# Kernel tuning notes

Hardware: AMD Instinct MI355X
Metric: run time of the kernel (lower is better)

## Reference

```python
import jax, jax.numpy as jnp
import numpy as np

H = 20  # hidden size (hardcoded in the torch module)

def setup_inputs() -> dict:
    key = jax.random.key(0)
    ks = jax.random.split(key, 7)
    s = 0.1  # keep activations in a sane range for tanh/sigmoid
    return {
        "x":     jax.random.normal(ks[0], (8192, 512, 12), dtype=jnp.float32),
        "w_ih":  jax.random.normal(ks[1], (4 * H, 12), dtype=jnp.float32) * s,
        "w_hh":  jax.random.normal(ks[2], (4 * H, H), dtype=jnp.float32) * s,
        "b_ih":  jax.random.normal(ks[3], (4 * H,), dtype=jnp.float32) * s,
        "b_hh":  jax.random.normal(ks[4], (4 * H,), dtype=jnp.float32) * s,
        "w_out": jax.random.normal(ks[5], (10, H), dtype=jnp.float32) * s,
        "b_out": jax.random.normal(ks[6], (10,), dtype=jnp.float32) * s,
    }

def reference(x, w_ih, w_hh, b_ih, b_hh, w_out, b_out):
    # x: [B, T, I]. Single-layer LSTM (PyTorch gate order i,f,g,o), zero init state,
    # then Linear on the last hidden state.
    B, T, _ = x.shape
    # Precompute input projections for all timesteps: [T, B, 4H]
    x_proj = jnp.einsum('bti,gi->tbg', x, w_ih) + (b_ih + b_hh)

    def step(carry, xt):
        h, c = carry                      # each [B, H]
        gates = xt + h @ w_hh.T           # [B, 4H]
        i, f, g, o = jnp.split(gates, 4, axis=-1)
        i = jax.nn.sigmoid(i)
        f = jax.nn.sigmoid(f)
        g = jnp.tanh(g)
        o = jax.nn.sigmoid(o)
        c = f * c + i * g
        h = o * jnp.tanh(c)
        return (h, c), None

    h0 = jnp.zeros((B, H), dtype=x.dtype)
    c0 = jnp.zeros((B, H), dtype=x.dtype)
    (h_last, _), _ = jax.lax.scan(step, (h0, c0), x_proj)
    # out = Linear(h_T): r_out[:, -1, :] == h_n for a single-layer LSTM
    return h_last @ w_out.T + b_out
```

## Files before the change

kernel.cpp:

```cpp
#include <hip/hip_runtime.h>

typedef _Float16 f16;
typedef f16 f16x8 __attribute__((ext_vector_type(8)));
typedef float f32x4 __attribute__((ext_vector_type(4)));

#define T_STEPS 512
#define INPUT   12
#define HID     20
#define KDIM    32
#define BSTRIDE 40
#define BATCH   16
#define WPB     5
#define BLOCK   (WPB * 64)

static __device__ __forceinline__ void block_barrier() {
    asm volatile("s_waitcnt lgkmcnt(0)\n\ts_barrier" ::: "memory");
}

static __device__ __forceinline__ float fast_sigmoid(float x) {
    float e = __builtin_amdgcn_exp2f(-1.4426950408889634f * x);
    return __builtin_amdgcn_rcpf(1.0f + e);
}
static __device__ __forceinline__ float fast_tanh(float x) {
    float e = __builtin_amdgcn_exp2f(2.8853900817779268f * x);
    return 1.0f - 2.0f * __builtin_amdgcn_rcpf(1.0f + e);
}

__global__ __launch_bounds__(BLOCK) void lstm_kernel(
    const float* __restrict__ x,
    const float* __restrict__ w_ih,
    const float* __restrict__ w_hh,
    const float* __restrict__ b_ih,
    const float* __restrict__ b_hh,
    const float* __restrict__ w_out,
    const float* __restrict__ b_out,
    float* __restrict__ out)
{
    __shared__ __align__(16) f16 Wc[80][KDIM];
    __shared__ __align__(16) f16 Bbuf[2][BATCH][BSTRIDE];

    const int tid  = threadIdx.x;
    const int wid  = tid >> 6;
    const int lane = tid & 63;
    const int col  = lane & 15;
    const int quad = lane >> 4;

    for (int i = tid; i < 80 * KDIM; i += BLOCK) {
        int n = i >> 5, k = i & 31;
        int g = n & 3;
        int u = 4 * (n >> 4) + ((n >> 2) & 3);
        int row = g * HID + u;
        float v = (k < INPUT) ? w_ih[row * INPUT + k] : w_hh[row * HID + (k - INPUT)];
        Wc[n][k] = (f16)v;
    }

    const int b = col;
    const int u = 4 * wid + quad;

    f32x4 cbias;
#pragma unroll
    for (int g = 0; g < 4; ++g)
        cbias[g] = b_ih[g * HID + u] + b_hh[g * HID + u];

    Bbuf[0][b][INPUT + u] = (f16)0.f;

    const bool xload = tid < BATCH * INPUT;
    const int  xb    = tid / INPUT;
    const int  xi    = tid % INPUT;
    const float* xptr = x + (size_t)(blockIdx.x * BATCH + xb) * (T_STEPS * INPUT) + xi;

    float q0 = 0.f, q1 = 0.f, q2 = 0.f, q3 = 0.f;
    if (xload) {
        Bbuf[0][xb][xi] = (f16)xptr[0];
        q0 = xptr[1 * INPUT];
        q1 = xptr[2 * INPUT];
        q2 = xptr[3 * INPUT];
        q3 = xptr[4 * INPUT];
    }
    __syncthreads();

    const f16x8 afragW = *(const f16x8*)&Wc[16 * wid + col][quad * 8];

    float cc = 0.f;

    auto step = [&](int pj, float& qreg, int tload) {
        f16x8 bfrag = *(const f16x8*)&Bbuf[pj][col][quad * 8];

        if (xload) Bbuf[pj ^ 1][xb][xi] = (f16)qreg;
        int tl = tload > T_STEPS - 1 ? T_STEPS - 1 : tload;
        if (xload) qreg = xptr[(size_t)tl * INPUT];

        f32x4 acc = __builtin_amdgcn_mfma_f32_16x16x32_f16(afragW, bfrag, cbias, 0, 0, 0);

        float ig = fast_sigmoid(acc[0]);
        float fg = fast_sigmoid(acc[1]);
        float gt = fast_tanh(acc[2]);
        float og = fast_sigmoid(acc[3]);
        cc = fg * cc + ig * gt;
        float h = og * fast_tanh(cc);

        Bbuf[pj ^ 1][b][INPUT + u] = (f16)h;
        block_barrier();
    };

#pragma unroll 1
    for (int t4 = 0; t4 < T_STEPS; t4 += 4) {
        step(0, q0, t4 + 5);
        step(1, q1, t4 + 6);
        step(0, q2, t4 + 7);
        step(1, q3, t4 + 8);
    }

    if (tid < BATCH * 10) {
        int ob = tid / 10, oo = tid % 10;
        float s = b_out[oo];
#pragma unroll
        for (int u2 = 0; u2 < HID; ++u2)
            s += w_out[oo * HID + u2] * (float)Bbuf[0][ob][INPUT + u2];
        out[(size_t)(blockIdx.x * BATCH + ob) * 10 + oo] = s;
    }
}

extern "C" void kernel_launch(void* const* d_in, const int* in_sizes, int n_in,
                              void* d_out, int out_size, void* d_ws, size_t ws_size,
                              hipStream_t stream) {
    const float* x     = (const float*)d_in[0];
    const float* w_ih  = (const float*)d_in[1];
    const float* w_hh  = (const float*)d_in[2];
    const float* b_ih  = (const float*)d_in[3];
    const float* b_hh  = (const float*)d_in[4];
    const float* w_out = (const float*)d_in[5];
    const float* b_out = (const float*)d_in[6];
    float* out = (float*)d_out;

    const int blocks = 8192 / BATCH;
    hipLaunchKernelGGL(lstm_kernel, dim3(blocks), dim3(BLOCK), 0, stream,
                       x, w_ih, w_hh, b_ih, b_hh, w_out, b_out, out);
}
```

Baseline: 424.5 us.

## Collapse LSTM block to one wavefront and fold activation scales into weights

Each block now runs a single 64-lane wavefront that issues all five gate MFMA tiles itself. This replaces the five-wave layout that needed a block-wide barrier every timestep, so only an LDS wait remains. The exp2 scaling constants are folded into the fp16 weights and biases, and the cell and hidden updates are merged algebraically so fewer reciprocals are needed. x loads become float4 vector loads. In exchange, each wave does five times the serial work per step and the block has a fifth of the threads, which may reduce latency hiding, and the rescaled fp16 weights change rounding slightly.

```diff
diff --git a/kernel.cpp b/kernel.cpp
--- a/kernel.cpp
+++ b/kernel.cpp
@@ -1,6 +1,7 @@
 #include <hip/hip_runtime.h>
 
 typedef _Float16 f16;
+typedef f16 f16x4 __attribute__((ext_vector_type(4)));
 typedef f16 f16x8 __attribute__((ext_vector_type(8)));
 typedef float f32x4 __attribute__((ext_vector_type(4)));
 
@@ -10,23 +11,13 @@
 #define KDIM    32
 #define BSTRIDE 40
 #define BATCH   16
-#define WPB     5
-#define BLOCK   (WPB * 64)
+#define NTILES  5
 
-static __device__ __forceinline__ void block_barrier() {
-    asm volatile("s_waitcnt lgkmcnt(0)\n\ts_barrier" ::: "memory");
+static __device__ __forceinline__ void lds_fence() {
+    asm volatile("s_waitcnt lgkmcnt(0)" ::: "memory");
 }
 
-static __device__ __forceinline__ float fast_sigmoid(float x) {
-    float e = __builtin_amdgcn_exp2f(-1.4426950408889634f * x);
-    return __builtin_amdgcn_rcpf(1.0f + e);
-}
-static __device__ __forceinline__ float fast_tanh(float x) {
-    float e = __builtin_amdgcn_exp2f(2.8853900817779268f * x);
-    return 1.0f - 2.0f * __builtin_amdgcn_rcpf(1.0f + e);
-}
-
-__global__ __launch_bounds__(BLOCK) void lstm_kernel(
+__global__ __launch_bounds__(64) void lstm_kernel(
     const float* __restrict__ x,
     const float* __restrict__ w_ih,
     const float* __restrict__ w_hh,
@@ -39,68 +30,96 @@
     __shared__ __align__(16) f16 Wc[80][KDIM];
     __shared__ __align__(16) f16 Bbuf[2][BATCH][BSTRIDE];
 
-    const int tid  = threadIdx.x;
-    const int wid  = tid >> 6;
-    const int lane = tid & 63;
-    const int col  = lane & 15;
+    const int lane = threadIdx.x;
+    const int b    = lane & 15;
     const int quad = lane >> 4;
 
-    for (int i = tid; i < 80 * KDIM; i += BLOCK) {
+    for (int i = lane; i < 80 * KDIM; i += 64) {
         int n = i >> 5, k = i & 31;
         int g = n & 3;
         int u = 4 * (n >> 4) + ((n >> 2) & 3);
         int row = g * HID + u;
         float v = (k < INPUT) ? w_ih[row * INPUT + k] : w_hh[row * HID + (k - INPUT)];
-        Wc[n][k] = (f16)v;
+        float sc = (g == 2) ? 2.8853900817779268f : -1.4426950408889634f;
+        Wc[n][k] = (f16)(v * sc);
     }
 
-    const int b = col;
-    const int u = 4 * wid + quad;
+    f32x4 cbias[NTILES];
+#pragma unroll
+    for (int w = 0; w < NTILES; ++w) {
+        int u = 4 * w + quad;
+#pragma unroll
+        for (int g = 0; g < 4; ++g) {
+            float sc = (g == 2) ? 2.8853900817779268f : -1.4426950408889634f;
+            cbias[w][g] = sc * (b_ih[g * HID + u] + b_hh[g * HID + u]);
+        }
+    }
 
-    f32x4 cbias;
 #pragma unroll
-    for (int g = 0; g < 4; ++g)
-        cbias[g] = b_ih[g * HID + u] + b_hh[g * HID + u];
+    for (int w = 0; w < NTILES; ++w)
+        Bbuf[0][b][INPUT + 4 * w + quad] = (f16)0.f;
 
-    Bbuf[0][b][INPUT + u] = (f16)0.f;
+    const bool xload = quad < 3;
+    const float* xptr = x + (size_t)(blockIdx.x * BATCH + b) * (T_STEPS * INPUT) + 4 * quad;
 
-    const bool xload = tid < BATCH * INPUT;
-    const int  xb    = tid / INPUT;
-    const int  xi    = tid % INPUT;
-    const float* xptr = x + (size_t)(blockIdx.x * BATCH + xb) * (T_STEPS * INPUT) + xi;
+    f32x4 q0 = {0.f,0.f,0.f,0.f}, q1 = q0, q2 = q0, q3 = q0;
+    if (xload) {
+        f32x4 x0 = *(const f32x4*)xptr;
+        f16x4 xc;
+#pragma unroll
+        for (int j = 0; j < 4; ++j) xc[j] = (f16)x0[j];
+        *(f16x4*)&Bbuf[0][b][4 * quad] = xc;
+        q0 = *(const f32x4*)(xptr + 1 * INPUT);
+        q1 = *(const f32x4*)(xptr + 2 * INPUT);
+        q2 = *(const f32x4*)(xptr + 3 * INPUT);
+        q3 = *(const f32x4*)(xptr + 4 * INPUT);
+    }
 
-    float q0 = 0.f, q1 = 0.f, q2 = 0.f, q3 = 0.f;
-    if (xload) {
-        Bbuf[0][xb][xi] = (f16)xptr[0];
-        q0 = xptr[1 * INPUT];
-        q1 = xptr[2 * INPUT];
-        q2 = xptr[3 * INPUT];
-        q3 = xptr[4 * INPUT];
-    }
-    __syncthreads();
+    lds_fence();
 
-    const f16x8 afragW = *(const f16x8*)&Wc[16 * wid + col][quad * 8];
+    f16x8 afrag[NTILES];
+#pragma unroll
+    for (int w = 0; w < NTILES; ++w)
+        afrag[w] = *(const f16x8*)&Wc[16 * w + b][quad * 8];
 
-    float cc = 0.f;
+    float cc[NTILES] = {0.f, 0.f, 0.f, 0.f, 0.f};
 
-    auto step = [&](int pj, float& qreg, int tload) {
-        f16x8 bfrag = *(const f16x8*)&Bbuf[pj][col][quad * 8];
+    auto step = [&](int pj, f32x4& qreg, int tload) {
+        lds_fence();
+        f16x8 bfrag = *(const f16x8*)&Bbuf[pj][b][quad * 8];
 
-        if (xload) Bbuf[pj ^ 1][xb][xi] = (f16)qreg;
-        int tl = tload > T_STEPS - 1 ? T_STEPS - 1 : tload;
-        if (xload) qreg = xptr[(size_t)tl * INPUT];
+        if (xload) {
+            f16x4 xc;
+#pragma unroll
+            for (int j = 0; j < 4; ++j) xc[j] = (f16)qreg[j];
+            *(f16x4*)&Bbuf[pj ^ 1][b][4 * quad] = xc;
+            int tl = tload < T_STEPS ? tload : T_STEPS - 1;
+            qreg = *(const f32x4*)(xptr + (size_t)tl * INPUT);
+        }
 
-        f32x4 acc = __builtin_amdgcn_mfma_f32_16x16x32_f16(afragW, bfrag, cbias, 0, 0, 0);
+        f32x4 acc[NTILES];
+#pragma unroll
+        for (int w = 0; w < NTILES; ++w)
+            acc[w] = __builtin_amdgcn_mfma_f32_16x16x32_f16(afrag[w], bfrag, cbias[w], 0, 0, 0);
 
-        float ig = fast_sigmoid(acc[0]);
-        float fg = fast_sigmoid(acc[1]);
-        float gt = fast_tanh(acc[2]);
-        float og = fast_sigmoid(acc[3]);
-        cc = fg * cc + ig * gt;
-        float h = og * fast_tanh(cc);
-
-        Bbuf[pj ^ 1][b][INPUT + u] = (f16)h;
-        block_barrier();
+#pragma unroll
+        for (int w = 0; w < NTILES; ++w) {
+            float ei = __builtin_amdgcn_exp2f(acc[w][0]);
+            float ef = __builtin_amdgcn_exp2f(acc[w][1]);
+            float eg = __builtin_amdgcn_exp2f(acc[w][2]);
+            float eo = __builtin_amdgcn_exp2f(acc[w][3]);
+            float Ai = 1.f + ei, Af = 1.f + ef, Ag = 1.f + eg, Ao = 1.f + eo;
+            float P  = Ai * Ag;
+            float rD = __builtin_amdgcn_rcpf(P * Af);
+            float nm = __builtin_fmaf(eg - 1.f, Af, cc[w] * P);
+            float c  = nm * rD;
+            cc[w] = c;
+            float et = __builtin_amdgcn_exp2f(2.8853900817779268f * c);
+            float At = 1.f + et;
+            float rM = __builtin_amdgcn_rcpf(At * Ao);
+            float h  = (et - 1.f) * rM;
+            Bbuf[pj ^ 1][b][INPUT + 4 * w + quad] = (f16)h;
+        }
     };
 
 #pragma unroll 1
@@ -111,8 +130,10 @@
         step(1, q3, t4 + 8);
     }
 
-    if (tid < BATCH * 10) {
-        int ob = tid / 10, oo = tid % 10;
+    lds_fence();
+
+    for (int i = lane; i < BATCH * 10; i += 64) {
+        int ob = i / 10, oo = i - 10 * ob;
         float s = b_out[oo];
 #pragma unroll
         for (int u2 = 0; u2 < HID; ++u2)
@@ -134,6 +155,6 @@
     float* out = (float*)d_out;
 
     const int blocks = 8192 / BATCH;
-    hipLaunchKernelGGL(lstm_kernel, dim3(blocks), dim3(BLOCK), 0, stream,
+    hipLaunchKernelGGL(lstm_kernel, dim3(blocks), dim3(64), 0, stream,
                        x, w_ih, w_hh, b_ih, b_hh, w_out, b_out, out);
 }
```

New measurement: 468.7 us. 1.1x slower.

## Process two batch groups per block and fold activation scaling into weights

Applied to the files above, without the earlier changes.

Each block now handles two independent 16-sequence groups. Two MFMAs and two gate computations share each barrier, and the block count is halved to 256. The log2e and 2·log2e scale factors are folded into the fp16 weights and biases. The gate math is then rewritten to combine the sigmoid and tanh reciprocals into fewer rcp calls. The aim is to amortise the per-step barrier latency and shorten the serial dependency chain, at the cost of fewer blocks (256 on a 256-CU part) and some precision risk from pre-scaled fp16 weights and combined products that could overflow.

```diff
diff --git a/kernel.cpp b/kernel.cpp
--- a/kernel.cpp
+++ b/kernel.cpp
@@ -10,20 +10,12 @@
 #define KDIM    32
 #define BSTRIDE 40
 #define BATCH   16
+#define NGRP    2
 #define WPB     5
 #define BLOCK   (WPB * 64)
 
 static __device__ __forceinline__ void block_barrier() {
     asm volatile("s_waitcnt lgkmcnt(0)\n\ts_barrier" ::: "memory");
-}
-
-static __device__ __forceinline__ float fast_sigmoid(float x) {
-    float e = __builtin_amdgcn_exp2f(-1.4426950408889634f * x);
-    return __builtin_amdgcn_rcpf(1.0f + e);
-}
-static __device__ __forceinline__ float fast_tanh(float x) {
-    float e = __builtin_amdgcn_exp2f(2.8853900817779268f * x);
-    return 1.0f - 2.0f * __builtin_amdgcn_rcpf(1.0f + e);
 }
 
 __global__ __launch_bounds__(BLOCK) void lstm_kernel(
@@ -37,13 +29,13 @@
     float* __restrict__ out)
 {
     __shared__ __align__(16) f16 Wc[80][KDIM];
-    __shared__ __align__(16) f16 Bbuf[2][BATCH][BSTRIDE];
+    __shared__ __align__(16) f16 Bbuf[NGRP][2][BATCH][BSTRIDE];
 
     const int tid  = threadIdx.x;
     const int wid  = tid >> 6;
     const int lane = tid & 63;
-    const int col  = lane & 15;
-    const int quad = lane >> 4;
+    const int c    = lane & 15;
+    const int q    = lane >> 4;
 
     for (int i = tid; i < 80 * KDIM; i += BLOCK) {
         int n = i >> 5, k = i & 31;
@@ -51,73 +43,110 @@
         int u = 4 * (n >> 4) + ((n >> 2) & 3);
         int row = g * HID + u;
         float v = (k < INPUT) ? w_ih[row * INPUT + k] : w_hh[row * HID + (k - INPUT)];
-        Wc[n][k] = (f16)v;
+        float sc = (g == 2) ? 2.8853900817779268f : -1.4426950408889634f;
+        Wc[n][k] = (f16)(v * sc);
     }
 
-    const int b = col;
-    const int u = 4 * wid + quad;
-
+    const int u = 4 * wid + q;
     f32x4 cbias;
 #pragma unroll
-    for (int g = 0; g < 4; ++g)
-        cbias[g] = b_ih[g * HID + u] + b_hh[g * HID + u];
+    for (int r = 0; r < 4; ++r) {
+        float sc = (r == 2) ? 2.8853900817779268f : -1.4426950408889634f;
+        cbias[r] = sc * (b_ih[r * HID + u] + b_hh[r * HID + u]);
+    }
 
-    Bbuf[0][b][INPUT + u] = (f16)0.f;
+    Bbuf[0][0][c][INPUT + u] = (f16)0.f;
+    Bbuf[1][0][c][INPUT + u] = (f16)0.f;
 
     const bool xload = tid < BATCH * INPUT;
     const int  xb    = tid / INPUT;
     const int  xi    = tid % INPUT;
-    const float* xptr = x + (size_t)(blockIdx.x * BATCH + xb) * (T_STEPS * INPUT) + xi;
+    const float* xpA = x + (size_t)(blockIdx.x * (BATCH * NGRP) + xb) * (T_STEPS * INPUT) + xi;
+    const float* xpB = xpA + (size_t)BATCH * (T_STEPS * INPUT);
 
-    float q0 = 0.f, q1 = 0.f, q2 = 0.f, q3 = 0.f;
+    float qA0 = 0.f, qA1 = 0.f, qA2 = 0.f, qA3 = 0.f;
+    float qB0 = 0.f, qB1 = 0.f, qB2 = 0.f, qB3 = 0.f;
     if (xload) {
-        Bbuf[0][xb][xi] = (f16)xptr[0];
-        q0 = xptr[1 * INPUT];
-        q1 = xptr[2 * INPUT];
-        q2 = xptr[3 * INPUT];
-        q3 = xptr[4 * INPUT];
+        Bbuf[0][0][xb][xi] = (f16)xpA[0];
+        Bbuf[1][0][xb][xi] = (f16)xpB[0];
+        qA0 = xpA[1 * INPUT]; qB0 = xpB[1 * INPUT];
+        qA1 = xpA[2 * INPUT]; qB1 = xpB[2 * INPUT];
+        qA2 = xpA[3 * INPUT]; qB2 = xpB[3 * INPUT];
+        qA3 = xpA[4 * INPUT]; qB3 = xpB[4 * INPUT];
     }
     __syncthreads();
 
-    const f16x8 afragW = *(const f16x8*)&Wc[16 * wid + col][quad * 8];
+    const f16x8 afragW = *(const f16x8*)&Wc[16 * wid + c][q * 8];
 
-    float cc = 0.f;
+    float ccA = 0.f, ccB = 0.f;
 
-    auto step = [&](int pj, float& qreg, int tload) {
-        f16x8 bfrag = *(const f16x8*)&Bbuf[pj][col][quad * 8];
+    auto step = [&](int pj, float& qA, float& qB, int tload) {
+        f16x8 bfA = *(const f16x8*)&Bbuf[0][pj][c][q * 8];
+        f16x8 bfB = *(const f16x8*)&Bbuf[1][pj][c][q * 8];
 
-        if (xload) Bbuf[pj ^ 1][xb][xi] = (f16)qreg;
-        int tl = tload > T_STEPS - 1 ? T_STEPS - 1 : tload;
-        if (xload) qreg = xptr[(size_t)tl * INPUT];
+        if (xload) {
+            Bbuf[0][pj ^ 1][xb][xi] = (f16)qA;
+            Bbuf[1][pj ^ 1][xb][xi] = (f16)qB;
+            int tl = tload < T_STEPS ? tload : T_STEPS - 1;
+            qA = xpA[(size_t)tl * INPUT];
+            qB = xpB[(size_t)tl * INPUT];
+        }
 
-        f32x4 acc = __builtin_amdgcn_mfma_f32_16x16x32_f16(afragW, bfrag, cbias, 0, 0, 0);
+        f32x4 aA = __builtin_amdgcn_mfma_f32_16x16x32_f16(afragW, bfA, cbias, 0, 0, 0);
+        f32x4 aB = __builtin_amdgcn_mfma_f32_16x16x32_f16(afragW, bfB, cbias, 0, 0, 0);
 
-        float ig = fast_sigmoid(acc[0]);
-        float fg = fast_sigmoid(acc[1]);
-        float gt = fast_tanh(acc[2]);
-        float og = fast_sigmoid(acc[3]);
-        cc = fg * cc + ig * gt;
-        float h = og * fast_tanh(cc);
+        {
+            float ei = __builtin_amdgcn_exp2f(aA[0]);
+            float ef = __builtin_amdgcn_exp2f(aA[1]);
+            float eg = __builtin_amdgcn_exp2f(aA[2]);
+            float eo = __builtin_amdgcn_exp2f(aA[3]);
+            float Ai = 1.f + ei, Af = 1.f + ef, Ag = 1.f + eg, Ao = 1.f + eo;
+            float P  = Ai * Ag;
+            float rD = __builtin_amdgcn_rcpf(P * Af);
+            float nm = __builtin_fmaf(eg - 1.f, Af, ccA * P);
+            float cn = nm * rD;
+            ccA = cn;
+            float et = __builtin_amdgcn_exp2f(2.8853900817779268f * cn);
+            float At = 1.f + et;
+            float rM = __builtin_amdgcn_rcpf(At * Ao);
+            Bbuf[0][pj ^ 1][c][INPUT + u] = (f16)((et - 1.f) * rM);
+        }
+        {
+            float ei = __builtin_amdgcn_exp2f(aB[0]);
+            float ef = __builtin_amdgcn_exp2f(aB[1]);
+            float eg = __builtin_amdgcn_exp2f(aB[2]);
+            float eo = __builtin_amdgcn_exp2f(aB[3]);
+            float Ai = 1.f + ei, Af = 1.f + ef, Ag = 1.f + eg, Ao = 1.f + eo;
+            float P  = Ai * Ag;
+            float rD = __builtin_amdgcn_rcpf(P * Af);
+            float nm = __builtin_fmaf(eg - 1.f, Af, ccB * P);
+            float cn = nm * rD;
+            ccB = cn;
+            float et = __builtin_amdgcn_exp2f(2.8853900817779268f * cn);
+            float At = 1.f + et;
+            float rM = __builtin_amdgcn_rcpf(At * Ao);
+            Bbuf[1][pj ^ 1][c][INPUT + u] = (f16)((et - 1.f) * rM);
+        }
 
-        Bbuf[pj ^ 1][b][INPUT + u] = (f16)h;
         block_barrier();
     };
 
 #pragma unroll 1
     for (int t4 = 0; t4 < T_STEPS; t4 += 4) {
-        step(0, q0, t4 + 5);
-        step(1, q1, t4 + 6);
-        step(0, q2, t4 + 7);
-        step(1, q3, t4 + 8);
+        step(0, qA0, qB0, t4 + 5);
+        step(1, qA1, qB1, t4 + 6);
+        step(0, qA2, qB2, t4 + 7);
+        step(1, qA3, qB3, t4 + 8);
     }
 
-    if (tid < BATCH * 10) {
-        int ob = tid / 10, oo = tid % 10;
+    {
+        int bb = tid / 10, oo = tid - 10 * bb;
+        int g  = bb >> 4, ob = bb & 15;
         float s = b_out[oo];
 #pragma unroll
         for (int u2 = 0; u2 < HID; ++u2)
-            s += w_out[oo * HID + u2] * (float)Bbuf[0][ob][INPUT + u2];
-        out[(size_t)(blockIdx.x * BATCH + ob) * 10 + oo] = s;
+            s += w_out[oo * HID + u2] * (float)Bbuf[g][0][ob][INPUT + u2];
+        out[(size_t)(blockIdx.x * (BATCH * NGRP) + bb) * 10 + oo] = s;
     }
 }
 
@@ -133,7 +162,7 @@
     const float* b_out = (const float*)d_in[6];
     float* out = (float*)d_out;
 
-    const int blocks = 8192 / BATCH;
+    const int blocks = 8192 / (BATCH * NGRP);
     hipLaunchKernelGGL(lstm_kernel, dim3(blocks), dim3(BLOCK), 0, stream,
                        x, w_ih, w_hh, b_ih, b_hh, w_out, b_out, out);
 }
```

New measurement: 430.7 us. About the same (+1.5%).
